# Kernel tuning notes

Measured on AMD Instinct MI355X. Metric: run time of the kernel, lower is better.

## Reference

```python
import jax, jax.numpy as jnp
import numpy as np

QMAX = 127.0  # int8 symmetric quantization range


def _quant_dequant(w):
    """Per-output-channel symmetric int8 fake quantization (weight-only),
    mimicking nn.quantized.Linear.from_float weight quantization."""
    scale = jnp.max(jnp.abs(w), axis=-1, keepdims=True) / QMAX
    scale = jnp.maximum(scale, 1e-8)
    q = jnp.clip(jnp.round(w / scale), -QMAX, QMAX)
    return q * scale


def setup_inputs() -> dict:
    key = jax.random.key(0)
    ks = jax.random.split(key, 7)
    B, S, D, F, E, NS = 2, 2048, 1024, 2048, 8, 1
    std = 1.0 / np.sqrt(D)
    x = jax.random.normal(ks[0], (B, S, D), dtype=jnp.float32)
    router_w = _quant_dequant(jax.random.normal(ks[1], (E, D), dtype=jnp.float32) * std)
    router_b = jnp.zeros((E,), dtype=jnp.float32)
    w_up = _quant_dequant(jax.random.normal(ks[2], (E, F, D), dtype=jnp.float32) * std)
    w_down = _quant_dequant(jax.random.normal(ks[3], (E, D, F), dtype=jnp.float32) / np.sqrt(F))
    shared_w_up = _quant_dequant(jax.random.normal(ks[4], (NS, F, D), dtype=jnp.float32) * std)
    shared_w_down = _quant_dequant(jax.random.normal(ks[5], (NS, D, F), dtype=jnp.float32) / np.sqrt(F))
    return {"x": x, "router_w": router_w, "router_b": router_b,
            "w_up": w_up, "w_down": w_down,
            "shared_w_up": shared_w_up, "shared_w_down": shared_w_down}


def reference(x, router_w, router_b, w_up, w_down, shared_w_up, shared_w_down):
    B, S, D = x.shape
    E = router_w.shape[0]
    TOPK = 2
    xt = x.reshape(-1, D)  # [T, D] tokens

    # Router (quantized linear) -> softmax -> top-k dispatch weights
    logits = xt @ router_w.T + router_b            # [T, E]
    probs = jax.nn.softmax(logits, axis=-1)        # [T, E]
    top_vals, top_idx = jax.lax.top_k(probs, TOPK)  # [T, K]
    top_vals = top_vals / jnp.sum(top_vals, axis=-1, keepdims=True)  # renormalize
    # combine[t, e] = routing weight of expert e for token t (0 if not selected)
    combine = jnp.sum(jax.nn.one_hot(top_idx, E, dtype=xt.dtype) * top_vals[..., None], axis=1)  # [T, E]

    # Routed experts: up -> SiLU -> down, computed densely then combined
    h = jnp.einsum('td,efd->tef', xt, w_up)        # [T, E, F]
    y = jnp.einsum('tef,edf->ted', jax.nn.silu(h), w_down)  # [T, E, D]
    out = jnp.einsum('ted,te->td', y, combine)     # [T, D]

    # Shared experts: always active, summed
    hs = jnp.einsum('td,sfd->tsf', xt, shared_w_up)          # [T, NS, F]
    out = out + jnp.einsum('tsf,sdf->td', jax.nn.silu(hs), shared_w_down)

    return out.reshape(B, S, D)
```

## Files before the change

kernel.cpp:

```cpp
#include <hip/hip_runtime.h>
#include <stdint.h>

typedef unsigned short u16;
typedef int i32x4 __attribute__((ext_vector_type(4)));

#define DDIM 1024
#define FDIM 2048
#define NEXP 8
#define RT_TILES 72
#define SHOFF 9216
#define RCAP 13312
#define NRT 104


__device__ inline float bf2f(u16 u) {
    union { unsigned int i; float f; } v; v.i = ((unsigned int)u) << 16; return v.f;
}
__device__ inline u16 f2bf(float f) {
    union { float f; unsigned int i; } v; v.f = f;
    unsigned int lsb = (v.i >> 16) & 1u;
    return (u16)((v.i + 0x7fffu + lsb) >> 16);
}
__device__ inline int q8(float v, float inv) {
    int x = (int)rintf(v * inv);
    return x < -127 ? -127 : (x > 127 ? 127 : x);
}

typedef const __attribute__((address_space(1))) void gas_void;
typedef __attribute__((address_space(3))) void las_void;
#define GLL16(g, l) __builtin_amdgcn_global_load_lds((gas_void*)(g), (las_void*)(l), 16, 0, 0)

__device__ inline int detect_inline(const u16* __restrict__ x, int* sh) {
    if (threadIdx.x == 0) *sh = 0;
    __syncthreads();
    const int per = 1024 / blockDim.x;
    int bad = 0;
    for (int i = 0; i < per; i++) {
        u16 v = x[threadIdx.x * per + i];
        if (((v >> 7) & 0xFF) >= 0x8F) bad++;
    }
    if (bad) atomicAdd(sh, bad);
    __syncthreads();
    return (*sh > 32) ? 1 : 0;
}

__global__ __launch_bounds__(256) void router_kernel(
    const void* __restrict__ x_, const void* __restrict__ rw_, const void* __restrict__ rb_,
    float* __restrict__ top_w, int* __restrict__ top_idx)
{
    __shared__ float rws[NEXP * DDIM];
    __shared__ int scnt;
    const int tid = threadIdx.x;
    const int flag = detect_inline((const u16*)x_, &scnt);

    if (!flag) {
        const ushort4* rwv = (const ushort4*)rw_;
        #pragma unroll
        for (int i = 0; i < 8; i++) {
            int idx = tid + i * 256;
            ushort4 h = rwv[idx];
            rws[idx * 4 + 0] = bf2f(h.x); rws[idx * 4 + 1] = bf2f(h.y);
            rws[idx * 4 + 2] = bf2f(h.z); rws[idx * 4 + 3] = bf2f(h.w);
        }
    } else {
        const float4* rwv = (const float4*)rw_;
        #pragma unroll
        for (int i = 0; i < 8; i++) {
            int idx = tid + i * 256;
            float4 f = rwv[idx];
            rws[idx * 4 + 0] = f.x; rws[idx * 4 + 1] = f.y;
            rws[idx * 4 + 2] = f.z; rws[idx * 4 + 3] = f.w;
        }
    }
    __syncthreads();

    const int wave = tid >> 6, lane = tid & 63;

    for (int sub = 0; sub < 4; sub++) {
        const int t = blockIdx.x * 16 + wave * 4 + sub;
        float xv[16];
        if (!flag) {
            const u16* xr = (const u16*)x_ + (size_t)t * DDIM + lane * 16;
            uint4 p0 = *(const uint4*)(xr);
            uint4 p1 = *(const uint4*)(xr + 8);
            #pragma unroll
            for (int d = 0; d < 8; d++) xv[d]     = bf2f(((const u16*)&p0)[d]);
            #pragma unroll
            for (int d = 0; d < 8; d++) xv[d + 8] = bf2f(((const u16*)&p1)[d]);
        } else {
            const float4* xr = (const float4*)((const float*)x_ + (size_t)t * DDIM + lane * 16);
            #pragma unroll
            for (int c = 0; c < 4; c++) {
                float4 f = xr[c];
                xv[c * 4 + 0] = f.x; xv[c * 4 + 1] = f.y;
                xv[c * 4 + 2] = f.z; xv[c * 4 + 3] = f.w;
            }
        }

        float acc[NEXP];
        #pragma unroll
        for (int e = 0; e < NEXP; e++) {
            const float* wr = &rws[e * DDIM + lane * 16];
            float s = 0.f;
            #pragma unroll
            for (int d = 0; d < 16; d++) s += xv[d] * wr[d];
            acc[e] = s;
        }
        #pragma unroll
        for (int e = 0; e < NEXP; e++) {
            #pragma unroll
            for (int off = 32; off > 0; off >>= 1)
                acc[e] += __shfl_xor(acc[e], off, 64);
        }
        if (lane == 0) {
            float lg[NEXP];
            #pragma unroll
            for (int e = 0; e < NEXP; e++) {
                float b = flag ? ((const float*)rb_)[e] : bf2f(((const u16*)rb_)[e]);
                lg[e] = acc[e] + b;
            }
            int i0 = 0;
            #pragma unroll
            for (int e = 1; e < NEXP; e++) if (lg[e] > lg[i0]) i0 = e;
            int i1 = (i0 == 0) ? 1 : 0;
            #pragma unroll
            for (int e = 0; e < NEXP; e++) if (e != i0 && lg[e] > lg[i1]) i1 = e;
            float e1 = __expf(lg[i1] - lg[i0]);
            float w0 = 1.f / (1.f + e1);
            float w1 = e1 / (1.f + e1);
            top_w[2 * t] = w0;  top_w[2 * t + 1] = w1;
            top_idx[2 * t] = i0; top_idx[2 * t + 1] = i1;
        }
    }
}

__global__ __launch_bounds__(1024) void rank_kernel(
    const u16* __restrict__ x, const int* __restrict__ top_idx,
    int* __restrict__ tok_rows, int* __restrict__ meta)
{
    __shared__ int wsum[16][NEXP];
    __shared__ int wbase[16][NEXP];
    __shared__ int scnt;
    const int tid = threadIdx.x, lane = tid & 63, wave = tid >> 6;

    const int flag = detect_inline(x, &scnt);
    if (tid == 0) meta[30] = flag;

    const int4* tp = (const int4*)(top_idx + tid * 8);
    int4 v0 = tp[0], v1 = tp[1];
    int e[8] = { v0.x, v0.y, v0.z, v0.w, v1.x, v1.y, v1.z, v1.w };

    int tcnt[NEXP];
    #pragma unroll
    for (int en = 0; en < NEXP; en++) tcnt[en] = 0;
    #pragma unroll
    for (int j = 0; j < 8; j++)
        #pragma unroll
        for (int en = 0; en < NEXP; en++) tcnt[en] += (e[j] == en);

    int excl[NEXP];
    #pragma unroll
    for (int en = 0; en < NEXP; en++) {
        int v = tcnt[en];
        #pragma unroll
        for (int off = 1; off < 64; off <<= 1) {
            int u = __shfl_up(v, off, 64);
            if (lane >= off) v += u;
        }
        excl[en] = v - tcnt[en];
        if (lane == 63) wsum[wave][en] = v;
    }
    __syncthreads();
    if (tid < NEXP) {
        int s = 0;
        for (int w = 0; w < 16; w++) { int c = wsum[w][tid]; wbase[w][tid] = s; s += c; }
        meta[tid] = s;
    }
    __syncthreads();
    if (tid == 0) {
        int b = 0;
        for (int en = 0; en < NEXP; en++) {
            meta[8 + en] = b;
            b += ((meta[en] + 127) >> 7) << 7;
        }
        meta[16] = b;
    }
    __syncthreads();

    int cur[NEXP];
    #pragma unroll
    for (int en = 0; en < NEXP; en++) cur[en] = meta[8 + en] + wbase[wave][en] + excl[en];

    int r[8];
    #pragma unroll
    for (int j = 0; j < 8; j++) {
        int rr = 0;
        #pragma unroll
        for (int en = 0; en < NEXP; en++)
            if (e[j] == en) { rr = cur[en]; cur[en] = rr + 1; }
        r[j] = rr;
    }
    int4* rp = (int4*)(tok_rows + tid * 8);
    rp[0] = make_int4(r[0], r[1], r[2], r[3]);
    rp[1] = make_int4(r[4], r[5], r[6], r[7]);
}

__global__ __launch_bounds__(128) void gather_q_kernel(
    const void* __restrict__ x_, const int* __restrict__ tok_rows,
    char* __restrict__ xq, float* __restrict__ sxa, const int* __restrict__ meta)
{
    __shared__ float red[128];
    const int t = blockIdx.x, tid = threadIdx.x;
    const int r0 = tok_rows[2 * t], r1 = tok_rows[2 * t + 1];

    float v[8];
    if (!meta[30]) {
        uint4 p = ((const uint4*)((const u16*)x_ + (size_t)t * DDIM))[tid];
        #pragma unroll
        for (int d = 0; d < 8; d++) v[d] = bf2f(((const u16*)&p)[d]);
    } else {
        const float4* xf = (const float4*)((const float*)x_ + (size_t)t * DDIM);
        float4 a = xf[2 * tid], b = xf[2 * tid + 1];
        v[0] = a.x; v[1] = a.y; v[2] = a.z; v[3] = a.w;
        v[4] = b.x; v[5] = b.y; v[6] = b.z; v[7] = b.w;
    }
    float m = 0.f;
    #pragma unroll
    for (int d = 0; d < 8; d++) m = fmaxf(m, fabsf(v[d]));
    red[tid] = m;
    __syncthreads();
    for (int s = 64; s > 0; s >>= 1) {
        if (tid < s) red[tid] = fmaxf(red[tid], red[tid + s]);
        __syncthreads();
    }
    const float mx = fmaxf(red[0], 1e-8f);
    const float inv = 127.f / mx;

    uint2 u;
    u.x = (unsigned)(q8(v[0], inv) & 255) | ((unsigned)(q8(v[1], inv) & 255) << 8) |
          ((unsigned)(q8(v[2], inv) & 255) << 16) | ((unsigned)(q8(v[3], inv) & 255) << 24);
    u.y = (unsigned)(q8(v[4], inv) & 255) | ((unsigned)(q8(v[5], inv) & 255) << 8) |
          ((unsigned)(q8(v[6], inv) & 255) << 16) | ((unsigned)(q8(v[7], inv) & 255) << 24);

    ((uint2*)(xq + (size_t)r0 * DDIM))[tid] = u;
    ((uint2*)(xq + (size_t)r1 * DDIM))[tid] = u;
    ((uint2*)(xq + (size_t)(SHOFF + t) * DDIM))[tid] = u;
    if (tid == 0) {
        float s = mx / 127.f;
        sxa[r0] = s; sxa[r1] = s; sxa[SHOFF + t] = s;
    }
}

template <int NCH>
__device__ inline void wquant_row(const char* src, char* dst, float* sc, int flag, int lane)
{
    float vals[NCH * 4];
    #pragma unroll
    for (int c = 0; c < NCH; c++) {
        if (flag) {
            float4 f = ((const float4*)src)[c * 64 + lane];
            vals[4 * c + 0] = f.x; vals[4 * c + 1] = f.y;
            vals[4 * c + 2] = f.z; vals[4 * c + 3] = f.w;
        } else {
            ushort4 h = ((const ushort4*)src)[c * 64 + lane];
            vals[4 * c + 0] = bf2f(h.x); vals[4 * c + 1] = bf2f(h.y);
            vals[4 * c + 2] = bf2f(h.z); vals[4 * c + 3] = bf2f(h.w);
        }
    }
    float m = 0.f;
    #pragma unroll
    for (int k = 0; k < NCH * 4; k++) m = fmaxf(m, fabsf(vals[k]));
    #pragma unroll
    for (int off = 32; off > 0; off >>= 1) m = fmaxf(m, __shfl_xor(m, off, 64));
    m = fmaxf(m, 1e-12f);
    if (lane == 0) *sc = m / 127.f;
    const float inv = 127.f / m;
    #pragma unroll
    for (int c = 0; c < NCH; c++) {
        unsigned u = (unsigned)(q8(vals[4 * c + 0], inv) & 255) |
                     ((unsigned)(q8(vals[4 * c + 1], inv) & 255) << 8) |
                     ((unsigned)(q8(vals[4 * c + 2], inv) & 255) << 16) |
                     ((unsigned)(q8(vals[4 * c + 3], inv) & 255) << 24);
        ((unsigned*)dst)[c * 64 + lane] = u;
    }
}

__global__ __launch_bounds__(256) void wquant_kernel(
    const void* __restrict__ w_up, const void* __restrict__ w_down,
    const void* __restrict__ sw_up, const void* __restrict__ sw_down,
    char* __restrict__ qup, char* __restrict__ qdn,
    float* __restrict__ su, float* __restrict__ sd, const int* __restrict__ meta)
{
    const int flag = meta[30];
    const int es = flag ? 4 : 2;
    const int tid = threadIdx.x, lane = tid & 63, wave = tid >> 6;
    const int R = blockIdx.x * 4 + wave;
    const int UPROWS = (NEXP + 1) * FDIM;

    if (R < UPROWS) {
        const void* base = (R < NEXP * FDIM) ? w_up : sw_up;
        size_t row = (R < NEXP * FDIM) ? (size_t)R : (size_t)(R - NEXP * FDIM);
        wquant_row<4>((const char*)base + row * DDIM * es, qup + (size_t)R * DDIM,
                      su + R, flag, lane);
    } else {
        const int R2 = R - UPROWS;
        const void* base = (R2 < NEXP * DDIM) ? w_down : sw_down;
        size_t row = (R2 < NEXP * DDIM) ? (size_t)R2 : (size_t)(R2 - NEXP * DDIM);
        wquant_row<8>((const char*)base + row * FDIM * es, qdn + (size_t)R2 * FDIM,
                      sd + R2, flag, lane);
    }
}

__global__ __launch_bounds__(256, 3) void moe_gemm_i8(
    const char* __restrict__ A, const char* __restrict__ Wq,
    const float* __restrict__ sa, const float* __restrict__ sw,
    u16* __restrict__ Cout, const int* __restrict__ meta, int N, int Kd, int act)
{
    const int L = blockIdx.y * gridDim.x + blockIdx.x;
    const int xcd = L & 7;
    const int j = L >> 3;
    const int rt = xcd * 13 + (j % 13);
    const int ct = j / 13;

    int e;
    if (rt >= RT_TILES) {
        e = NEXP;
    } else {
        const int r0t = rt * 128;
        if (r0t >= meta[16]) return;
        e = 0;
        #pragma unroll
        for (int i = 1; i < NEXP; i++) if (r0t >= meta[8 + i]) e = i;
        if (r0t >= meta[8 + e] + meta[e]) return;
    }
    const char* Wb = Wq + (size_t)(e * N + ct * 128) * Kd;
    const float* swb = sw + e * N + ct * 128;

    __shared__ char As[2][128 * 64];
    __shared__ char Bs[2][128 * 64];

    const int tid = threadIdx.x;
    const int wave = tid >> 6, lane = tid & 63;
    const int wm = (wave >> 1) * 64;
    const int wn = (wave & 1) * 64;
    const int l16 = lane & 15;
    const int q = lane >> 4;
    const int srow = tid >> 2;
    const int qs = ((tid & 3) - ((tid >> 3) & 3)) & 3;
    const int slot = (q + (l16 >> 1)) & 3;

    const char* Ag = A + (size_t)(rt * 128 + srow) * Kd + qs * 16;
    const char* Bg = Wb + (size_t)srow * Kd + qs * 16;
    const size_t half = (size_t)64 * Kd;

    i32x4 acc[4][4] = {};

    GLL16(Ag,        &As[0][wave * 1024]);
    GLL16(Ag + half, &As[0][4096 + wave * 1024]);
    GLL16(Bg,        &Bs[0][wave * 1024]);
    GLL16(Bg + half, &Bs[0][4096 + wave * 1024]);
    __syncthreads();

    int cur = 0;
    for (int kk = 0; kk < Kd; kk += 64) {
        if (kk + 64 < Kd) {
            const int nb = cur ^ 1;
            GLL16(Ag + kk + 64,        &As[nb][wave * 1024]);
            GLL16(Ag + half + kk + 64, &As[nb][4096 + wave * 1024]);
            GLL16(Bg + kk + 64,        &Bs[nb][wave * 1024]);
            GLL16(Bg + half + kk + 64, &Bs[nb][4096 + wave * 1024]);
        }
        i32x4 af[4], bf[4];
        #pragma unroll
        for (int i = 0; i < 4; i++)
            af[i] = *(const i32x4*)&As[cur][(wm + i * 16 + l16) * 64 + slot * 16];
        #pragma unroll
        for (int j2 = 0; j2 < 4; j2++)
            bf[j2] = *(const i32x4*)&Bs[cur][(wn + j2 * 16 + l16) * 64 + slot * 16];
        #pragma unroll
        for (int i = 0; i < 4; i++)
            #pragma unroll
            for (int j2 = 0; j2 < 4; j2++)
                acc[i][j2] = __builtin_amdgcn_mfma_i32_16x16x64_i8(af[i], bf[j2], acc[i][j2], 0, 0, 0);
        __syncthreads();
        cur ^= 1;
    }

    float sal[4][4];
    #pragma unroll
    for (int i = 0; i < 4; i++)
        #pragma unroll
        for (int rr = 0; rr < 4; rr++)
            sal[i][rr] = sa[rt * 128 + wm + i * 16 + q * 4 + rr];
    float swl[4];
    #pragma unroll
    for (int j2 = 0; j2 < 4; j2++) swl[j2] = swb[wn + j2 * 16 + l16];

    u16* Crow = Cout + (size_t)(rt * 128) * N + ct * 128;
    #pragma unroll
    for (int i = 0; i < 4; i++) {
        #pragma unroll
        for (int j2 = 0; j2 < 4; j2++) {
            #pragma unroll
            for (int rr = 0; rr < 4; rr++) {
                const int row = wm + i * 16 + q * 4 + rr;
                const int col = wn + j2 * 16 + l16;
                float v = (float)acc[i][j2][rr] * sal[i][rr] * swl[j2];
                if (act) v = v / (1.f + __expf(-v));
                Crow[(size_t)row * N + col] = f2bf(v);
            }
        }
    }
}

__global__ __launch_bounds__(256) void hquant_kernel(
    const u16* __restrict__ hg, char* __restrict__ h8, float* __restrict__ sh,
    const int* __restrict__ meta)
{
    const int r = blockIdx.x;
    if (r >= meta[16] && r < SHOFF) return;
    __shared__ float red[256];
    const int tid = threadIdx.x;
    const u16* row = hg + (size_t)r * FDIM;
    uint4 p = ((const uint4*)row)[tid];
    float v[8];
    #pragma unroll
    for (int d = 0; d < 8; d++) v[d] = bf2f(((const u16*)&p)[d]);
    float m = 0.f;
    #pragma unroll
    for (int d = 0; d < 8; d++) m = fmaxf(m, fabsf(v[d]));
    red[tid] = m;
    __syncthreads();
    for (int s = 128; s > 0; s >>= 1) {
        if (tid < s) red[tid] = fmaxf(red[tid], red[tid + s]);
        __syncthreads();
    }
    const float mx = fmaxf(red[0], 1e-8f);
    const float inv = 127.f / mx;
    if (tid == 0) sh[r] = mx / 127.f;
    uint2 u;
    u.x = (unsigned)(q8(v[0], inv) & 255) | ((unsigned)(q8(v[1], inv) & 255) << 8) |
          ((unsigned)(q8(v[2], inv) & 255) << 16) | ((unsigned)(q8(v[3], inv) & 255) << 24);
    u.y = (unsigned)(q8(v[4], inv) & 255) | ((unsigned)(q8(v[5], inv) & 255) << 8) |
          ((unsigned)(q8(v[6], inv) & 255) << 16) | ((unsigned)(q8(v[7], inv) & 255) << 24);
    ((uint2*)(h8 + (size_t)r * FDIM))[tid] = u;
}

__global__ __launch_bounds__(256) void combine_kernel(
    const u16* __restrict__ yg, const float* __restrict__ top_w,
    const int* __restrict__ tok_rows, void* __restrict__ out_, const int* __restrict__ meta)
{
    const int t = blockIdx.x;
    const int r0 = tok_rows[2 * t], r1 = tok_rows[2 * t + 1];
    const float w0 = top_w[2 * t], w1 = top_w[2 * t + 1];
    const int d = threadIdx.x * 4;
    ushort4 y0 = *(const ushort4*)(yg + (size_t)r0 * DDIM + d);
    ushort4 y1 = *(const ushort4*)(yg + (size_t)r1 * DDIM + d);
    ushort4 ys = *(const ushort4*)(yg + (size_t)(SHOFF + t) * DDIM + d);
    float o0 = w0 * bf2f(y0.x) + w1 * bf2f(y1.x) + bf2f(ys.x);
    float o1 = w0 * bf2f(y0.y) + w1 * bf2f(y1.y) + bf2f(ys.y);
    float o2 = w0 * bf2f(y0.z) + w1 * bf2f(y1.z) + bf2f(ys.z);
    float o3 = w0 * bf2f(y0.w) + w1 * bf2f(y1.w) + bf2f(ys.w);
    if (!meta[30]) {
        ushort4 o; o.x = f2bf(o0); o.y = f2bf(o1); o.z = f2bf(o2); o.w = f2bf(o3);
        *(ushort4*)((u16*)out_ + (size_t)t * DDIM + d) = o;
    } else {
        float4 o; o.x = o0; o.y = o1; o.z = o2; o.w = o3;
        *(float4*)((float*)out_ + (size_t)t * DDIM + d) = o;
    }
}

extern "C" void kernel_launch(void* const* d_in, const int* in_sizes, int n_in,
                              void* d_out, int out_size, void* d_ws, size_t ws_size,
                              hipStream_t stream) {
    const void* x       = d_in[0];
    const void* rw      = d_in[1];
    const void* rb      = d_in[2];
    const void* w_up    = d_in[3];
    const void* w_down  = d_in[4];
    const void* sw_up   = d_in[5];
    const void* sw_down = d_in[6];

    const int T = in_sizes[0] / DDIM;

    char* ws = (char*)d_ws;
    int*   meta     = (int*)ws;
    float* top_w    = (float*)(ws + 1024);
    int*   top_idx  = (int*)(ws + 1024 + 8 * T);
    int*   tok_rows = (int*)(ws + 1024 + 16 * T);
    size_t off = 131072;
    u16*  yg = (u16*)(ws + off);
    char* xq = (char*)(ws + off);
    off += (size_t)RCAP * DDIM * 2;
    u16*  hg = (u16*)(ws + off);
    off += (size_t)RCAP * FDIM * 2;
    char* h8 = (char*)(ws + off);
    off += (size_t)RCAP * FDIM;
    char* qup = (char*)(ws + off);
    off += (size_t)(NEXP + 1) * FDIM * DDIM;
    char* qdn = (char*)(ws + off);
    off += (size_t)(NEXP + 1) * DDIM * FDIM;
    float* sxa = (float*)(ws + off); off += (size_t)RCAP * 4;
    float* sh  = (float*)(ws + off); off += (size_t)RCAP * 4;
    float* su  = (float*)(ws + off); off += (size_t)(NEXP + 1) * FDIM * 4;
    float* sd  = (float*)(ws + off); off += (size_t)(NEXP + 1) * DDIM * 4;

    router_kernel<<<T / 16, 256, 0, stream>>>(x, rw, rb, top_w, top_idx);
    rank_kernel<<<1, 1024, 0, stream>>>((const u16*)x, top_idx, tok_rows, meta);
    gather_q_kernel<<<T, 128, 0, stream>>>(x, tok_rows, xq, sxa, meta);
    wquant_kernel<<<((NEXP + 1) * (FDIM + DDIM)) / 4, 256, 0, stream>>>(
        w_up, w_down, sw_up, sw_down, qup, qdn, su, sd, meta);

    moe_gemm_i8<<<dim3(FDIM / 128, NRT), 256, 0, stream>>>(
        xq, qup, sxa, su, hg, meta, FDIM, DDIM, 1);
    hquant_kernel<<<RCAP, 256, 0, stream>>>(hg, h8, sh, meta);
    moe_gemm_i8<<<dim3(DDIM / 128, NRT), 256, 0, stream>>>(
        h8, qdn, sh, sd, yg, meta, DDIM, FDIM, 0);
    combine_kernel<<<T, 256, 0, stream>>>(yg, top_w, tok_rows, d_out, meta);
}
```

Before: 324.6 us.

## Widen int8 MoE GEMM tile to 128x256 and quantize three weight rows per wave

The int8 MoE GEMM now computes a 128x256 output tile per block, with each wave holding a 64x128 accumulator. This doubles reuse of the A tile and halves the number of column blocks. Occupancy drops to 2 blocks per CU, and B shared memory doubles. The weight-quantization kernel now has each wave process three rows, interleaving their loads and shuffle reductions for more memory-level parallelism. That kernel's grid shrinks to match.

```diff
diff --git a/kernel.cpp b/kernel.cpp
--- a/kernel.cpp
+++ b/kernel.cpp
@@ -252,36 +252,52 @@
 }
 
 template <int NCH>
-__device__ inline void wquant_row(const char* src, char* dst, float* sc, int flag, int lane)
-{
-    float vals[NCH * 4];
-    #pragma unroll
-    for (int c = 0; c < NCH; c++) {
-        if (flag) {
-            float4 f = ((const float4*)src)[c * 64 + lane];
-            vals[4 * c + 0] = f.x; vals[4 * c + 1] = f.y;
-            vals[4 * c + 2] = f.z; vals[4 * c + 3] = f.w;
-        } else {
-            ushort4 h = ((const ushort4*)src)[c * 64 + lane];
-            vals[4 * c + 0] = bf2f(h.x); vals[4 * c + 1] = bf2f(h.y);
-            vals[4 * c + 2] = bf2f(h.z); vals[4 * c + 3] = bf2f(h.w);
-        }
-    }
-    float m = 0.f;
-    #pragma unroll
-    for (int k = 0; k < NCH * 4; k++) m = fmaxf(m, fabsf(vals[k]));
-    #pragma unroll
-    for (int off = 32; off > 0; off >>= 1) m = fmaxf(m, __shfl_xor(m, off, 64));
-    m = fmaxf(m, 1e-12f);
-    if (lane == 0) *sc = m / 127.f;
-    const float inv = 127.f / m;
-    #pragma unroll
-    for (int c = 0; c < NCH; c++) {
-        unsigned u = (unsigned)(q8(vals[4 * c + 0], inv) & 255) |
-                     ((unsigned)(q8(vals[4 * c + 1], inv) & 255) << 8) |
-                     ((unsigned)(q8(vals[4 * c + 2], inv) & 255) << 16) |
-                     ((unsigned)(q8(vals[4 * c + 3], inv) & 255) << 24);
-        ((unsigned*)dst)[c * 64 + lane] = u;
+__device__ inline void wquant_rows3(const char* s0, const char* s1, const char* s2,
+                                    char* dst, float* sc, int flag, int lane)
+{
+    const char* s[3] = { s0, s1, s2 };
+    float vals[3][NCH * 4];
+    #pragma unroll
+    for (int r = 0; r < 3; r++) {
+        #pragma unroll
+        for (int c = 0; c < NCH; c++) {
+            if (flag) {
+                float4 f = ((const float4*)s[r])[c * 64 + lane];
+                vals[r][4 * c + 0] = f.x; vals[r][4 * c + 1] = f.y;
+                vals[r][4 * c + 2] = f.z; vals[r][4 * c + 3] = f.w;
+            } else {
+                ushort4 h = ((const ushort4*)s[r])[c * 64 + lane];
+                vals[r][4 * c + 0] = bf2f(h.x); vals[r][4 * c + 1] = bf2f(h.y);
+                vals[r][4 * c + 2] = bf2f(h.z); vals[r][4 * c + 3] = bf2f(h.w);
+            }
+        }
+    }
+    float m[3];
+    #pragma unroll
+    for (int r = 0; r < 3; r++) {
+        float mm = 0.f;
+        #pragma unroll
+        for (int k = 0; k < NCH * 4; k++) mm = fmaxf(mm, fabsf(vals[r][k]));
+        m[r] = mm;
+    }
+    #pragma unroll
+    for (int off = 32; off > 0; off >>= 1) {
+        #pragma unroll
+        for (int r = 0; r < 3; r++) m[r] = fmaxf(m[r], __shfl_xor(m[r], off, 64));
+    }
+    #pragma unroll
+    for (int r = 0; r < 3; r++) {
+        m[r] = fmaxf(m[r], 1e-12f);
+        if (lane == 0) sc[r] = m[r] / 127.f;
+        const float inv = 127.f / m[r];
+        #pragma unroll
+        for (int c = 0; c < NCH; c++) {
+            unsigned u = (unsigned)(q8(vals[r][4 * c + 0], inv) & 255) |
+                         ((unsigned)(q8(vals[r][4 * c + 1], inv) & 255) << 8) |
+                         ((unsigned)(q8(vals[r][4 * c + 2], inv) & 255) << 16) |
+                         ((unsigned)(q8(vals[r][4 * c + 3], inv) & 255) << 24);
+            ((unsigned*)dst)[r * (NCH * 64) + c * 64 + lane] = u;
+        }
     }
 }
 
@@ -292,35 +308,46 @@
     float* __restrict__ su, float* __restrict__ sd, const int* __restrict__ meta)
 {
     const int flag = meta[30];
-    const int es = flag ? 4 : 2;
-    const int tid = threadIdx.x, lane = tid & 63, wave = tid >> 6;
-    const int R = blockIdx.x * 4 + wave;
-    const int UPROWS = (NEXP + 1) * FDIM;
-
-    if (R < UPROWS) {
-        const void* base = (R < NEXP * FDIM) ? w_up : sw_up;
-        size_t row = (R < NEXP * FDIM) ? (size_t)R : (size_t)(R - NEXP * FDIM);
-        wquant_row<4>((const char*)base + row * DDIM * es, qup + (size_t)R * DDIM,
-                      su + R, flag, lane);
+    const size_t es = flag ? 4 : 2;
+    const int lane = threadIdx.x & 63;
+    const int g = blockIdx.x * 4 + (threadIdx.x >> 6);
+    const int UPG = (NEXP + 1) * FDIM / 3;
+
+    if (g < UPG) {
+        const int R0 = g * 3;
+        const char* s[3];
+        #pragma unroll
+        for (int r = 0; r < 3; r++) {
+            const int R = R0 + r;
+            s[r] = (R < NEXP * FDIM)
+                 ? (const char*)w_up  + (size_t)R * DDIM * es
+                 : (const char*)sw_up + (size_t)(R - NEXP * FDIM) * DDIM * es;
+        }
+        wquant_rows3<4>(s[0], s[1], s[2], qup + (size_t)R0 * DDIM, su + R0, flag, lane);
     } else {
-        const int R2 = R - UPROWS;
-        const void* base = (R2 < NEXP * DDIM) ? w_down : sw_down;
-        size_t row = (R2 < NEXP * DDIM) ? (size_t)R2 : (size_t)(R2 - NEXP * DDIM);
-        wquant_row<8>((const char*)base + row * FDIM * es, qdn + (size_t)R2 * FDIM,
-                      sd + R2, flag, lane);
-    }
-}
-
-__global__ __launch_bounds__(256, 3) void moe_gemm_i8(
+        const int R0 = (g - UPG) * 3;
+        const char* s[3];
+        #pragma unroll
+        for (int r = 0; r < 3; r++) {
+            const int R = R0 + r;
+            s[r] = (R < NEXP * DDIM)
+                 ? (const char*)w_down  + (size_t)R * FDIM * es
+                 : (const char*)sw_down + (size_t)(R - NEXP * DDIM) * FDIM * es;
+        }
+        wquant_rows3<8>(s[0], s[1], s[2], qdn + (size_t)R0 * FDIM, sd + R0, flag, lane);
+    }
+}
+
+__global__ __launch_bounds__(256, 2) void moe_gemm_i8(
     const char* __restrict__ A, const char* __restrict__ Wq,
     const float* __restrict__ sa, const float* __restrict__ sw,
     u16* __restrict__ Cout, const int* __restrict__ meta, int N, int Kd, int act)
 {
     const int L = blockIdx.y * gridDim.x + blockIdx.x;
     const int xcd = L & 7;
-    const int j = L >> 3;
-    const int rt = xcd * 13 + (j % 13);
-    const int ct = j / 13;
+    const int jj = L >> 3;
+    const int rt = xcd * 13 + (jj % 13);
+    const int ct = jj / 13;
 
     int e;
     if (rt >= RT_TILES) {
@@ -333,58 +360,60 @@
         for (int i = 1; i < NEXP; i++) if (r0t >= meta[8 + i]) e = i;
         if (r0t >= meta[8 + e] + meta[e]) return;
     }
-    const char* Wb = Wq + (size_t)(e * N + ct * 128) * Kd;
-    const float* swb = sw + e * N + ct * 128;
+    const char* Wb = Wq + (size_t)(e * N + ct * 256) * Kd;
+    const float* swb = sw + e * N + ct * 256;
 
     __shared__ char As[2][128 * 64];
-    __shared__ char Bs[2][128 * 64];
+    __shared__ char Bs[2][256 * 64];
 
     const int tid = threadIdx.x;
     const int wave = tid >> 6, lane = tid & 63;
     const int wm = (wave >> 1) * 64;
-    const int wn = (wave & 1) * 64;
+    const int wn = (wave & 1) * 128;
     const int l16 = lane & 15;
     const int q = lane >> 4;
-    const int srow = tid >> 2;
-    const int qs = ((tid & 3) - ((tid >> 3) & 3)) & 3;
     const int slot = (q + (l16 >> 1)) & 3;
 
-    const char* Ag = A + (size_t)(rt * 128 + srow) * Kd + qs * 16;
-    const char* Bg = Wb + (size_t)srow * Kd + qs * 16;
-    const size_t half = (size_t)64 * Kd;
-
-    i32x4 acc[4][4] = {};
-
-    GLL16(Ag,        &As[0][wave * 1024]);
-    GLL16(Ag + half, &As[0][4096 + wave * 1024]);
-    GLL16(Bg,        &Bs[0][wave * 1024]);
-    GLL16(Bg + half, &Bs[0][4096 + wave * 1024]);
+    const int rsub = lane >> 2;
+    const int qs = ((lane & 3) - ((lane >> 3) & 3)) & 3;
+
+    const char* Ag = A + (size_t)(rt * 128 + wave * 16 + rsub) * Kd + qs * 16;
+    const char* Bg = Wb + (size_t)(wave * 16 + rsub) * Kd + qs * 16;
+    const size_t rstep = (size_t)64 * Kd;
+
+    i32x4 acc[4][8] = {};
+
+#define STAGE(buf, off) do { \
+        GLL16(Ag + (off),             &As[buf][wave * 1024]); \
+        GLL16(Ag + (off) + rstep,     &As[buf][4096 + wave * 1024]); \
+        GLL16(Bg + (off),             &Bs[buf][wave * 1024]); \
+        GLL16(Bg + (off) + rstep,     &Bs[buf][4096 + wave * 1024]); \
+        GLL16(Bg + (off) + 2 * rstep, &Bs[buf][8192 + wave * 1024]); \
+        GLL16(Bg + (off) + 3 * rstep, &Bs[buf][12288 + wave * 1024]); \
+    } while (0)
+
+    STAGE(0, 0);
     __syncthreads();
 
     int cur = 0;
     for (int kk = 0; kk < Kd; kk += 64) {
-        if (kk + 64 < Kd) {
-            const int nb = cur ^ 1;
-            GLL16(Ag + kk + 64,        &As[nb][wave * 1024]);
-            GLL16(Ag + half + kk + 64, &As[nb][4096 + wave * 1024]);
-            GLL16(Bg + kk + 64,        &Bs[nb][wave * 1024]);
-            GLL16(Bg + half + kk + 64, &Bs[nb][4096 + wave * 1024]);
-        }
-        i32x4 af[4], bf[4];
+        if (kk + 64 < Kd) STAGE(cur ^ 1, kk + 64);
+        i32x4 af[4], bf[8];
         #pragma unroll
         for (int i = 0; i < 4; i++)
             af[i] = *(const i32x4*)&As[cur][(wm + i * 16 + l16) * 64 + slot * 16];
         #pragma unroll
-        for (int j2 = 0; j2 < 4; j2++)
-            bf[j2] = *(const i32x4*)&Bs[cur][(wn + j2 * 16 + l16) * 64 + slot * 16];
+        for (int j = 0; j < 8; j++)
+            bf[j] = *(const i32x4*)&Bs[cur][(wn + j * 16 + l16) * 64 + slot * 16];
         #pragma unroll
         for (int i = 0; i < 4; i++)
             #pragma unroll
-            for (int j2 = 0; j2 < 4; j2++)
-                acc[i][j2] = __builtin_amdgcn_mfma_i32_16x16x64_i8(af[i], bf[j2], acc[i][j2], 0, 0, 0);
+            for (int j = 0; j < 8; j++)
+                acc[i][j] = __builtin_amdgcn_mfma_i32_16x16x64_i8(af[i], bf[j], acc[i][j], 0, 0, 0);
         __syncthreads();
         cur ^= 1;
     }
+#undef STAGE
 
     float sal[4][4];
     #pragma unroll
@@ -392,20 +421,20 @@
         #pragma unroll
         for (int rr = 0; rr < 4; rr++)
             sal[i][rr] = sa[rt * 128 + wm + i * 16 + q * 4 + rr];
-    float swl[4];
-    #pragma unroll
-    for (int j2 = 0; j2 < 4; j2++) swl[j2] = swb[wn + j2 * 16 + l16];
-
-    u16* Crow = Cout + (size_t)(rt * 128) * N + ct * 128;
+    float swl[8];
+    #pragma unroll
+    for (int j = 0; j < 8; j++) swl[j] = swb[wn + j * 16 + l16];
+
+    u16* Crow = Cout + (size_t)(rt * 128) * N + ct * 256;
     #pragma unroll
     for (int i = 0; i < 4; i++) {
         #pragma unroll
-        for (int j2 = 0; j2 < 4; j2++) {
+        for (int j = 0; j < 8; j++) {
             #pragma unroll
             for (int rr = 0; rr < 4; rr++) {
                 const int row = wm + i * 16 + q * 4 + rr;
-                const int col = wn + j2 * 16 + l16;
-                float v = (float)acc[i][j2][rr] * sal[i][rr] * swl[j2];
+                const int col = wn + j * 16 + l16;
+                float v = (float)acc[i][j][rr] * sal[i][rr] * swl[j];
                 if (act) v = v / (1.f + __expf(-v));
                 Crow[(size_t)row * N + col] = f2bf(v);
             }
@@ -508,13 +537,13 @@
     router_kernel<<<T / 16, 256, 0, stream>>>(x, rw, rb, top_w, top_idx);
     rank_kernel<<<1, 1024, 0, stream>>>((const u16*)x, top_idx, tok_rows, meta);
     gather_q_kernel<<<T, 128, 0, stream>>>(x, tok_rows, xq, sxa, meta);
-    wquant_kernel<<<((NEXP + 1) * (FDIM + DDIM)) / 4, 256, 0, stream>>>(
+    wquant_kernel<<<2304, 256, 0, stream>>>(
         w_up, w_down, sw_up, sw_down, qup, qdn, su, sd, meta);
 
-    moe_gemm_i8<<<dim3(FDIM / 128, NRT), 256, 0, stream>>>(
+    moe_gemm_i8<<<dim3(FDIM / 256, NRT), 256, 0, stream>>>(
         xq, qup, sxa, su, hg, meta, FDIM, DDIM, 1);
     hquant_kernel<<<RCAP, 256, 0, stream>>>(hg, h8, sh, meta);
-    moe_gemm_i8<<<dim3(DDIM / 128, NRT), 256, 0, stream>>>(
+    moe_gemm_i8<<<dim3(DDIM / 256, NRT), 256, 0, stream>>>(
         h8, qdn, sh, sd, yg, meta, DDIM, FDIM, 0);
     combine_kernel<<<T, 256, 0, stream>>>(yg, top_w, tok_rows, d_out, meta);
 }
```

Result: no change. 327.5 us (+0.9%).
